# Kernel tuning notes

Hardware: AMD Instinct MI355X
Metric: run time of the kernel (lower is better)

The kernel has to match this reference:

```python
import jax, jax.numpy as jnp
import numpy as np

N = 50000      # nodes
E = 800000     # edges (before self loops)
H = 8          # heads in first n_layer-1 GATConv layers
C = 16         # per-head channels (hidden/heads)
HID = 128      # hidden_channels
IN = 128       # in_dim
OUT = 10       # out_dim
G = 64         # number of graphs in batch
EPS = 1e-5     # BatchNorm eps
SLOPE = 0.2    # GATConv leaky_relu negative slope


def _gat_conv(x, src, dst, W, att_src, att_dst, bias, heads, ch):
    # x: [N, HID]; W: [HID, heads*ch]; att_*: [heads, ch]; bias: [heads*ch]
    h = (x @ W).reshape(N, heads, ch)                       # [N, h, c]
    a_src = jnp.sum(h * att_src, axis=-1)                   # [N, h]
    a_dst = jnp.sum(h * att_dst, axis=-1)                   # [N, h]
    e = jax.nn.leaky_relu(a_src[src] + a_dst[dst], SLOPE)   # [E', h]
    # numerically stable segment softmax over incoming edges of each dst node
    e = e - jax.ops.segment_max(e, dst, num_segments=N)[dst]
    ee = jnp.exp(e)
    denom = jax.ops.segment_sum(ee, dst, num_segments=N)[dst]
    alpha = ee / denom                                      # [E', h]
    out = jax.ops.segment_sum(h[src] * alpha[..., None], dst, num_segments=N)
    return out.reshape(N, heads * ch) + bias                # [N, heads*ch]


def _bn(x, gamma, beta):
    # PyG BatchNorm in training mode: batch stats over node dim (biased var)
    m = jnp.mean(x, axis=0)
    v = jnp.var(x, axis=0)
    return (x - m) * jax.lax.rsqrt(v + EPS) * gamma + beta


def setup_inputs() -> dict:
    key = jax.random.key(0)
    ks = jax.random.split(key, 24)
    s = 0.05
    inp = {
        "x": jax.random.normal(ks[0], (N, IN), jnp.float32),
        "edge_index": jax.random.randint(ks[1], (2, E), 0, N, jnp.int64),
        "cycle_index": jax.random.randint(ks[2], (2, 1000), 0, N, jnp.int64),
        "batch": jnp.sort(jax.random.randint(ks[3], (N,), 0, G, jnp.int64)),
        "W_emb": jax.random.normal(ks[4], (IN, HID), jnp.float32) * s,
        "b_emb": jnp.zeros((HID,), jnp.float32),
        "conv_W": jax.random.normal(ks[5], (2, HID, H * C), jnp.float32) * s,
        "conv_att_src": jax.random.normal(ks[6], (2, H, C), jnp.float32) * s,
        "conv_att_dst": jax.random.normal(ks[7], (2, H, C), jnp.float32) * s,
        "conv_b": jnp.zeros((2, H * C), jnp.float32),
        "conv2_W": jax.random.normal(ks[8], (HID, HID), jnp.float32) * s,
        "conv2_att_src": jax.random.normal(ks[9], (1, HID), jnp.float32) * s,
        "conv2_att_dst": jax.random.normal(ks[10], (1, HID), jnp.float32) * s,
        "conv2_b": jnp.zeros((HID,), jnp.float32),
        "bn_gamma": jnp.ones((3, HID), jnp.float32),
        "bn_beta": jnp.zeros((3, HID), jnp.float32),
        "lin1_W": jax.random.normal(ks[11], (HID, HID), jnp.float32) * s,
        "lin1_b": jnp.zeros((HID,), jnp.float32),
        "lin2_W": jax.random.normal(ks[12], (HID, HID), jnp.float32) * s,
        "lin2_b": jnp.zeros((HID,), jnp.float32),
        "lin3_W": jax.random.normal(ks[13], (HID, OUT), jnp.float32) * s,
        "lin3_b": jnp.zeros((OUT,), jnp.float32),
    }
    return inp


def reference(x, edge_index, cycle_index, batch, W_emb, b_emb, conv_W,
              conv_att_src, conv_att_dst, conv_b, conv2_W, conv2_att_src,
              conv2_att_dst, conv2_b, bn_gamma, bn_beta, lin1_W, lin1_b,
              lin2_W, lin2_b, lin3_W, lin3_b):
    # GATConv default add_self_loops=True
    loops = jnp.arange(N, dtype=edge_index.dtype)
    src = jnp.concatenate([edge_index[0], loops])
    dst = jnp.concatenate([edge_index[1], loops])

    h = x @ W_emb + b_emb  # dropout(p=0) is identity
    for i in range(3):
        if i < 2:
            c = _gat_conv(h, src, dst, conv_W[i], conv_att_src[i],
                          conv_att_dst[i], conv_b[i], H, C)
        else:
            c = _gat_conv(h, src, dst, conv2_W, conv2_att_src,
                          conv2_att_dst, conv2_b, 1, HID)
        h = jax.nn.relu(_bn(c, bn_gamma[i], bn_beta[i])) + h

    # global mean pool over graphs
    sums = jax.ops.segment_sum(h, batch, num_segments=G)
    cnts = jax.ops.segment_sum(jnp.ones((N, 1), h.dtype), batch, num_segments=G)
    pooled = sums / jnp.maximum(cnts, 1.0)

    out = jax.nn.relu(pooled @ lin1_W + lin1_b)
    out = jax.nn.relu(out @ lin2_W + lin2_b)
    return out @ lin3_W + lin3_b
```

## Files before the change

### kernel.cpp

```cpp
#include <hip/hip_runtime.h>


#define NN   50000
#define NE   800000
#define NET  (NE + NN)
#define HD   128
#define NG   64
#define NB   196
#define NBN  391
#define NCH  20
#define NTILE 3321
#define PSZ  6250

typedef unsigned short u16;
typedef __attribute__((ext_vector_type(8))) short short8;
typedef __attribute__((ext_vector_type(4))) float f32x4;

#define O_WEMB 0
#define O_BEMB 16384
#define O_CW   16512
#define O_CAS  49280
#define O_CAD  49536
#define O_CB   49792
#define O_C2W  50048
#define O_C2AS 66432
#define O_C2AD 66560
#define O_C2B  66688
#define O_BNG  66816
#define O_BNB  67200
#define O_L1W  67584
#define O_L1B  83968
#define O_L2W  84096
#define O_L2B  100480
#define O_L3W  100608
#define O_L3B  101888
#define NPAR   101898

__device__ int   g_f32flag;
__device__ __align__(16) u16 g_x [NN*HD];
__device__ __align__(16) u16 g_par[NPAR];
__device__ int   g_src[NE], g_dst[NE], g_batch[NN];
__device__ __align__(16) float g_h[NN*HD];
__device__ __align__(16) u16 g_hb[NN*HD];
__device__ __align__(16) u16 g_hw[NN*HD];
__device__ __align__(16) u16 g_c[NN*HD];
__device__ float g_asrc[NN*8];
__device__ float g_adst[NN*8];
__device__ int   g_rowptr[NN+1];
__device__ int   g_cursor[NN];
__device__ int   g_bsum[NB], g_boff[NB];
__device__ int   g_csr[NET];
__device__ float g_bnp1[NBN*HD], g_bnp2[NBN*HD];
__device__ float g_scl[HD], g_shf[HD];
__device__ int   g_gcnt[NG], g_goff[NG];
__device__ __align__(16) float g_poolp[NG*NCH*HD];
__device__ __align__(16) u16 g_WT[4][HD*HD];

__device__ __forceinline__ float b2f(u16 u) {
    unsigned v = ((unsigned)u) << 16; float f; __builtin_memcpy(&f, &v, 4); return f;
}
__device__ __forceinline__ u16 f2b(float f) {
    unsigned v; __builtin_memcpy(&v, &f, 4);
    return (u16)((v + 0x7fffu + ((v >> 16) & 1u)) >> 16);
}

__device__ __forceinline__ int probe_f32(const void* xp) {
    const u16* p = (const u16*)xp;
    int ex = (p[threadIdx.x & 63] >> 7) & 0xff;
    return __ballot(ex >= 0x93) != 0ULL;
}
__device__ __forceinline__ int probe_i64(const void* eip) {
    const int* q = (const int*)eip;
    return __ballot(q[2*(threadIdx.x & 63) + 1] != 0) == 0ULL;
}

__device__ __forceinline__ int block_incl_scan(int v, int* lds4) {
    int t = threadIdx.x, lane = t & 63, w = t >> 6;
    #pragma unroll
    for (int d = 1; d < 64; d <<= 1) {
        int o = __shfl_up(v, d);
        if (lane >= d) v += o;
    }
    if (lane == 63) lds4[w] = v;
    __syncthreads();
    if (w == 0 && lane < 4) {
        int s = lds4[lane];
        #pragma unroll
        for (int d = 1; d < 4; d <<= 1) {
            int o = __shfl_up(s, d);
            if (lane >= d) s += o;
        }
        lds4[lane] = s;
    }
    __syncthreads();
    if (w > 0) v += lds4[w-1];
    return v;
}

__global__ void k_convx(const void* xp) {
    int gi = blockIdx.x*256 + threadIdx.x;
    int f32 = probe_f32(xp);
    if (gi == 0) g_f32flag = f32;
    if (gi < NN) g_cursor[gi] = 1;
    int i = gi*4;
    if (f32) {
        float4 v = *(const float4*)((const float*)xp + i);
        ushort4 o = { f2b(v.x), f2b(v.y), f2b(v.z), f2b(v.w) };
        *(ushort4*)&g_x[i] = o;
    } else {
        *(ushort4*)&g_x[i] = *(const ushort4*)((const u16*)xp + i);
    }
}
struct P18 { const void* p[18]; int off[18]; int n[18]; };
__global__ void k_convpar(P18 a, const void* xp) {
    int f32 = probe_f32(xp);
    for (int t = 0; t < 18; ++t) {
        const void* s = a.p[t]; int off = a.off[t], n = a.n[t];
        for (int i = blockIdx.x*256 + threadIdx.x; i < n; i += 64*256)
            g_par[off+i] = f32 ? f2b(((const float*)s)[i]) : ((const u16*)s)[i];
    }
}
__global__ void k_convidx(const void* ei, const void* ba) {
    int i64 = probe_i64(ei);
    int e = blockIdx.x*256 + threadIdx.x;
    if (e < NE) {
        int s, d;
        if (i64) { s = (int)((const long long*)ei)[e]; d = (int)((const long long*)ei)[NE + e]; }
        else     { s = ((const int*)ei)[e];            d = ((const int*)ei)[NE + e]; }
        g_src[e] = s; g_dst[e] = d;
        atomicAdd(&g_cursor[d], 1);
    }
    if (e < NN)
        g_batch[e] = i64 ? (int)((const long long*)ba)[e] : ((const int*)ba)[e];
}

__global__ void k_blocksum() {
    int i = blockIdx.x*256 + threadIdx.x;
    int v = (i < NN) ? g_cursor[i] : 0;
    #pragma unroll
    for (int d = 32; d; d >>= 1) v += __shfl_down(v, d);
    __shared__ int lds[4];
    if ((threadIdx.x & 63) == 0) lds[threadIdx.x >> 6] = v;
    __syncthreads();
    if (threadIdx.x == 0) g_bsum[blockIdx.x] = lds[0]+lds[1]+lds[2]+lds[3];
}
__global__ void k_misc() {
    int b = blockIdx.x;
    if (b < 256) {
        int which = b >> 6;
        int poff = which==0 ? O_WEMB : which==1 ? O_CW : which==2 ? (O_CW+16384) : O_C2W;
        int idx = (b & 63)*256 + threadIdx.x;
        int n = idx >> 7, k = idx & 127;
        g_WT[which][n*HD + k] = g_par[poff + k*HD + n];
    } else if (b == 256) {
        __shared__ int lds[4];
        int t = threadIdx.x;
        int v = (t < NB) ? g_bsum[t] : 0;
        int incl = block_incl_scan(v, lds);
        if (t < NB) g_boff[t] = incl - v;
    } else {
        __shared__ int off[NG+1];
        int g = threadIdx.x;
        if (g <= NG) {
            int lo = 0, hi = NN;
            while (lo < hi) { int mid = (lo+hi) >> 1; if (g_batch[mid] < g) lo = mid+1; else hi = mid; }
            off[g] = lo;
        }
        __syncthreads();
        if (g < NG) { g_goff[g] = off[g]; g_gcnt[g] = off[g+1] - off[g]; }
    }
}
__global__ void k_downsweep() {
    __shared__ int lds[4];
    int i = blockIdx.x*256 + threadIdx.x;
    int c = (i < NN) ? g_cursor[i] : 0;
    int incl = block_incl_scan(c, lds);
    int base = g_boff[blockIdx.x];
    if (i < NN) {
        g_rowptr[i+1] = base + incl;
        g_cursor[i]   = base + incl - c;
    }
    if (i == 0) g_rowptr[0] = 0;
}

__global__ void k_scatter() {
    int part = blockIdx.x & 7;
    int e = (blockIdx.x >> 3)*256 + threadIdx.x;
    if (e >= NET) return;
    int s, d;
    if (e < NE) { s = g_src[e]; d = g_dst[e]; } else { s = d = e - NE; }
    if (d / PSZ != part) return;
    int pos = atomicAdd(&g_cursor[d], 1);
    g_csr[pos] = s;
}

__global__ __launch_bounds__(256) void k_gemm(int asel, int wsel, int biasoff,
                                              int outmode, int nrows,
                                              int asoff, int adoff, int heads,
                                              int bnfuse) {
    __shared__ __align__(16) u16 wt[HD*136];
    __shared__ float s_scl[HD], s_shf[HD];
    const u16* A = asel ? g_hb : g_x;
    const u16* WTg = g_WT[wsel];
    int t = threadIdx.x;
    #pragma unroll
    for (int i = 0; i < 8; ++i) {
        int e = (t + i*256) * 8;
        int n = e >> 7, k = e & 127;
        *(uint4*)&wt[n*136 + k] = *(const uint4*)&WTg[e];
    }
    if (bnfuse && t < HD) { s_scl[t] = g_scl[t]; s_shf[t] = g_shf[t]; }
    __syncthreads();
    int lane = t & 63, wave = t >> 6;
    int m16 = lane & 15, q = lane >> 4;
    int row0 = blockIdx.x*128 + wave*32;
    f32x4 acc[2][8];
    #pragma unroll
    for (int a = 0; a < 2; ++a)
        #pragma unroll
        for (int b = 0; b < 8; ++b) acc[a][b] = (f32x4){0.f,0.f,0.f,0.f};
    #pragma unroll
    for (int kc = 0; kc < 4; ++kc) {
        short8 af[2];
        #pragma unroll
        for (int rt = 0; rt < 2; ++rt) {
            int r = row0 + rt*16 + m16; if (r > nrows-1) r = nrows-1;
            int base = r*HD + kc*32 + q*8;
            if (bnfuse) {
                short8 cv = *(const short8*)&g_c[base];
                float4 h0 = *(const float4*)&g_h[base];
                float4 h1 = *(const float4*)&g_h[base+4];
                float nh[8];
                #pragma unroll
                for (int k2 = 0; k2 < 8; ++k2) {
                    int ch = kc*32 + q*8 + k2;
                    float hv = (k2 < 4) ? (&h0.x)[k2] : (&h1.x)[k2-4];
                    float v = fmaxf(b2f((u16)cv[k2])*s_scl[ch] + s_shf[ch], 0.f) + hv;
                    nh[k2] = v;
                    af[rt][k2] = (short)f2b(v);
                }
                float4 o0 = {nh[0],nh[1],nh[2],nh[3]};
                float4 o1 = {nh[4],nh[5],nh[6],nh[7]};
                *(float4*)&g_h[base]   = o0;
                *(float4*)&g_h[base+4] = o1;
            } else {
                af[rt] = *(const short8*)&A[base];
            }
        }
        #pragma unroll
        for (int ct = 0; ct < 8; ++ct) {
            short8 bf = *(const short8*)&wt[(ct*16 + m16)*136 + kc*32 + q*8];
            acc[0][ct] = __builtin_amdgcn_mfma_f32_16x16x32_bf16(af[0], bf, acc[0][ct], 0,0,0);
            acc[1][ct] = __builtin_amdgcn_mfma_f32_16x16x32_bf16(af[1], bf, acc[1][ct], 0,0,0);
        }
    }
    #pragma unroll
    for (int rt = 0; rt < 2; ++rt)
        #pragma unroll
        for (int reg = 0; reg < 4; ++reg) {
            int r = row0 + rt*16 + q*4 + reg;
            if (r < nrows) {
                #pragma unroll
                for (int ct = 0; ct < 8; ++ct) {
                    int c = ct*16 + m16;
                    float v = acc[rt][ct][reg];
                    if (biasoff >= 0) v += b2f(g_par[biasoff + c]);
                    if (outmode == 0) { g_h[r*HD+c] = v; g_hb[r*HD+c] = f2b(v); }
                    else              { g_hw[r*HD+c] = f2b(v); }
                }
            }
        }
    if (asoff >= 0) {
        #pragma unroll
        for (int rt = 0; rt < 2; ++rt)
            #pragma unroll
            for (int reg = 0; reg < 4; ++reg) {
                float v[8], u[8];
                #pragma unroll
                for (int ct = 0; ct < 8; ++ct) {
                    float w = acc[rt][ct][reg];
                    v[ct] = w * b2f(g_par[asoff + ct*16 + m16]);
                    u[ct] = w * b2f(g_par[adoff + ct*16 + m16]);
                }
                #pragma unroll
                for (int d = 1; d < 16; d <<= 1)
                    #pragma unroll
                    for (int ct = 0; ct < 8; ++ct) {
                        v[ct] += __shfl_xor(v[ct], d);
                        u[ct] += __shfl_xor(u[ct], d);
                    }
                int r = row0 + rt*16 + q*4 + reg;
                if (m16 == 0 && r < nrows) {
                    if (heads == 8) {
                        #pragma unroll
                        for (int h = 0; h < 8; ++h) {
                            g_asrc[r*8 + h] = v[h];
                            g_adst[r*8 + h] = u[h];
                        }
                    } else {
                        float sv = 0.f, su = 0.f;
                        #pragma unroll
                        for (int ct = 0; ct < 8; ++ct) { sv += v[ct]; su += u[ct]; }
                        g_asrc[r] = sv; g_adst[r] = su;
                    }
                }
            }
    }
}

__global__ __launch_bounds__(256) void k_flash(int boff, int heads, int hs) {
    int node = blockIdx.x*4 + (threadIdx.x >> 6);
    int lane = threadIdx.x & 63;
    int c0 = lane*2;
    int head = c0 >> hs;
    float ad = g_adst[node*heads + head];
    int beg = g_rowptr[node], end = g_rowptr[node+1];
    float l = 0.f, o0 = 0.f, o1 = 0.f;
    int j = beg;
    for (; j + 8 <= end; j += 8) {
        int s[8]; float av[8]; unsigned w[8];
        #pragma unroll
        for (int k = 0; k < 8; ++k) s[k] = g_csr[j+k];
        #pragma unroll
        for (int k = 0; k < 8; ++k) av[k] = g_asrc[s[k]*heads + head];
        #pragma unroll
        for (int k = 0; k < 8; ++k) w[k] = *(const unsigned*)&g_hw[s[k]*HD + c0];
        #pragma unroll
        for (int k = 0; k < 8; ++k) {
            float e = av[k] + ad;
            e = fmaxf(e, 0.2f*e);
            float p = __expf(fminf(e, 30.f));
            l  += p;
            o0 += p*b2f((u16)(w[k] & 0xffff));
            o1 += p*b2f((u16)(w[k] >> 16));
        }
    }
    for (; j + 4 <= end; j += 4) {
        int s[4]; float av[4]; unsigned w[4];
        #pragma unroll
        for (int k = 0; k < 4; ++k) s[k] = g_csr[j+k];
        #pragma unroll
        for (int k = 0; k < 4; ++k) av[k] = g_asrc[s[k]*heads + head];
        #pragma unroll
        for (int k = 0; k < 4; ++k) w[k] = *(const unsigned*)&g_hw[s[k]*HD + c0];
        #pragma unroll
        for (int k = 0; k < 4; ++k) {
            float e = av[k] + ad;
            e = fmaxf(e, 0.2f*e);
            float p = __expf(fminf(e, 30.f));
            l  += p;
            o0 += p*b2f((u16)(w[k] & 0xffff));
            o1 += p*b2f((u16)(w[k] >> 16));
        }
    }
    for (; j < end; ++j) {
        int s = g_csr[j];
        float e = g_asrc[s*heads + head] + ad;
        e = fmaxf(e, 0.2f*e);
        float p = __expf(fminf(e, 30.f));
        unsigned w = *(const unsigned*)&g_hw[s*HD + c0];
        l  += p;
        o0 += p*b2f((u16)(w & 0xffff));
        o1 += p*b2f((u16)(w >> 16));
    }
    float inv = 1.f/l;
    ushort2 o = { f2b(o0*inv + b2f(g_par[boff + c0])),
                  f2b(o1*inv + b2f(g_par[boff + c0 + 1])) };
    *(ushort2*)&g_c[node*HD + c0] = o;
}

__global__ void k_bnstats() {
    int t = threadIdx.x; int ch = t & 127, r0 = t >> 7;
    int base = blockIdx.x*128;
    float s = 0.f, q = 0.f;
    for (int i = r0; i < 128; i += 2) {
        int n = base + i;
        if (n < NN) { float v = b2f(g_c[n*HD + ch]); s += v; q += v*v; }
    }
    __shared__ float sS[256], sQ[256];
    sS[t] = s; sQ[t] = q; __syncthreads();
    if (t < 128) {
        g_bnp1[blockIdx.x*HD + t] = sS[t] + sS[t+128];
        g_bnp2[blockIdx.x*HD + t] = sQ[t] + sQ[t+128];
    }
}
__global__ void k_bnfinal(int goff, int boff) {
    int ch = blockIdx.x, t = threadIdx.x;
    float s = 0.f, q = 0.f;
    for (int b = t; b < NBN; b += 64) { s += g_bnp1[b*HD + ch]; q += g_bnp2[b*HD + ch]; }
    #pragma unroll
    for (int d = 32; d; d >>= 1) { s += __shfl_down(s, d); q += __shfl_down(q, d); }
    if (t == 0) {
        float mean = s / (float)NN;
        float var  = fmaxf(q / (float)NN - mean*mean, 0.f);
        float sc = b2f(g_par[goff + ch]) * rsqrtf(var + 1e-5f);
        g_scl[ch] = sc;
        g_shf[ch] = b2f(g_par[boff + ch]) - mean*sc;
    }
}

__global__ void k_pool() {
    int g = blockIdx.x / NCH, c = blockIdx.x - g*NCH;
    int cnt = g_gcnt[g], off = g_goff[g];
    int step = (cnt + NCH - 1) / NCH;
    int r0 = c*step, r1 = min(cnt, r0 + step);
    int t = threadIdx.x;
    int ch = (t & 31) * 4;
    int rr = t >> 5;
    float sc0 = g_scl[ch], sc1 = g_scl[ch+1], sc2 = g_scl[ch+2], sc3 = g_scl[ch+3];
    float sf0 = g_shf[ch], sf1 = g_shf[ch+1], sf2 = g_shf[ch+2], sf3 = g_shf[ch+3];
    float4 s = {0.f,0.f,0.f,0.f};
    for (int i = r0 + rr; i < r1; i += 8) {
        int base = (off + i)*HD + ch;
        ushort4 cv = *(const ushort4*)&g_c[base];
        float4 hv = *(const float4*)&g_h[base];
        s.x += fmaxf(b2f(cv.x)*sc0 + sf0, 0.f) + hv.x;
        s.y += fmaxf(b2f(cv.y)*sc1 + sf1, 0.f) + hv.y;
        s.z += fmaxf(b2f(cv.z)*sc2 + sf2, 0.f) + hv.z;
        s.w += fmaxf(b2f(cv.w)*sc3 + sf3, 0.f) + hv.w;
    }
    __shared__ float4 sh[256];
    sh[t] = s; __syncthreads();
    if (t < 32) {
        float4 a = sh[t];
        #pragma unroll
        for (int k = 1; k < 8; ++k) {
            float4 b = sh[t + k*32];
            a.x += b.x; a.y += b.y; a.z += b.z; a.w += b.w;
        }
        *(float4*)&g_poolp[(g*NCH + c)*HD + ch] = a;
    }
}

__global__ void k_head(void* outB) {
    __shared__ float pl[HD], h1[HD], h2[HD];
    int g = blockIdx.x, t = threadIdx.x;
    float s = 0.f;
    for (int c = 0; c < NCH; ++c) s += g_poolp[(g*NCH + c)*HD + t];
    pl[t] = s / fmaxf((float)g_gcnt[g], 1.f);
    __syncthreads();
    float acc = b2f(g_par[O_L1B + t]);
    for (int k = 0; k < HD; ++k) acc += pl[k] * b2f(g_par[O_L1W + k*HD + t]);
    h1[t] = fmaxf(acc, 0.f);
    __syncthreads();
    acc = b2f(g_par[O_L2B + t]);
    for (int k = 0; k < HD; ++k) acc += h1[k] * b2f(g_par[O_L2W + k*HD + t]);
    h2[t] = fmaxf(acc, 0.f);
    __syncthreads();
    if (t < 10) {
        acc = b2f(g_par[O_L3B + t]);
        for (int k = 0; k < HD; ++k) acc += h2[k] * b2f(g_par[O_L3W + k*10 + t]);
        if (g_f32flag) ((float*)outB)[g*10 + t] = acc;
        else           ((u16*)outB)[g*10 + t] = f2b(acc);
    }
}

extern "C" void kernel_launch(void* const* d_in, const int* in_sizes, int n_in,
                              void* d_out, int out_size, void* d_ws, size_t ws_size,
                              hipStream_t stream) {
    const void* x     = d_in[0];
    const void* ei    = d_in[1];
    const void* batch = d_in[3];

    k_convx<<<6250, 256, 0, stream>>>(x);
    P18 a;
    const int srcidx[18] = {4,5,6,7,8,9,10,11,12,13,14,15,16,17,18,19,20,21};
    const int offs[18] = {O_WEMB,O_BEMB,O_CW,O_CAS,O_CAD,O_CB,O_C2W,O_C2AS,O_C2AD,
                          O_C2B,O_BNG,O_BNB,O_L1W,O_L1B,O_L2W,O_L2B,O_L3W,O_L3B};
    const int lens[18] = {16384,128,32768,256,256,256,16384,128,128,128,384,384,
                          16384,128,16384,128,1280,10};
    for (int t = 0; t < 18; ++t) { a.p[t] = d_in[srcidx[t]]; a.off[t] = offs[t]; a.n[t] = lens[t]; }
    k_convpar<<<64, 256, 0, stream>>>(a, x);
    k_convidx<<<3125, 256, 0, stream>>>(ei, batch);

    k_blocksum<<<NB, 256, 0, stream>>>();
    k_misc<<<258, 256, 0, stream>>>();
    k_downsweep<<<NB, 256, 0, stream>>>();
    k_scatter<<<NTILE*8, 256, 0, stream>>>();

    k_gemm<<<391, 256, 0, stream>>>(0, 0, O_BEMB, 0, NN, -1, -1, 0, 0);

    for (int L = 0; L < 3; ++L) {
        int heads = (L < 2) ? 8 : 1;
        int hs    = (L < 2) ? 4 : 7;
        int as    = (L < 2) ? O_CAS + L*128 : O_C2AS;
        int ad    = (L < 2) ? O_CAD + L*128 : O_C2AD;
        int cb    = (L < 2) ? O_CB  + L*128 : O_C2B;
        k_gemm<<<391, 256, 0, stream>>>(1, L+1, -1, 1, NN, as, ad, heads, L > 0 ? 1 : 0);
        k_flash<<<12500, 256, 0, stream>>>(cb, heads, hs);
        k_bnstats<<<NBN, 256, 0, stream>>>();
        k_bnfinal<<<128, 64, 0, stream>>>(O_BNG + L*HD, O_BNB + L*HD);
    }

    k_pool<<<NG*NCH, 256, 0, stream>>>();
    k_head<<<NG, 128, 0, stream>>>(d_out);
}
```

Before: 552.9 us.

## Keep residual stream in bf16, merge param conversion kernel, defer src load

Removes the fp32 residual buffer g_h and keeps the running node features only in bf16 (g_hb). The fused BN+ReLU+residual step in the GEMM and the pooling kernel now read and write bf16. This halves residual memory traffic and drops the duplicate fp32 stores. It also folds the parameter conversion kernel into the input conversion kernel to save a launch, and loads src in the scatter kernel only after the partition check. Keeping the residual in bf16 adds rounding error that builds up across layers.

```diff
diff --git a/kernel.cpp b/kernel.cpp
--- a/kernel.cpp
+++ b/kernel.cpp
@@ -40,7 +40,6 @@
 __device__ __align__(16) u16 g_x [NN*HD];
 __device__ __align__(16) u16 g_par[NPAR];
 __device__ int   g_src[NE], g_dst[NE], g_batch[NN];
-__device__ __align__(16) float g_h[NN*HD];
 __device__ __align__(16) u16 g_hb[NN*HD];
 __device__ __align__(16) u16 g_hw[NN*HD];
 __device__ __align__(16) u16 g_c[NN*HD];
@@ -97,7 +96,8 @@
     return v;
 }
 
-__global__ void k_convx(const void* xp) {
+struct P18 { const void* p[18]; int off[18]; int n[18]; };
+__global__ void k_convx(const void* xp, P18 a) {
     int gi = blockIdx.x*256 + threadIdx.x;
     int f32 = probe_f32(xp);
     if (gi == 0) g_f32flag = f32;
@@ -110,14 +110,12 @@
     } else {
         *(ushort4*)&g_x[i] = *(const ushort4*)((const u16*)xp + i);
     }
-}
-struct P18 { const void* p[18]; int off[18]; int n[18]; };
-__global__ void k_convpar(P18 a, const void* xp) {
-    int f32 = probe_f32(xp);
-    for (int t = 0; t < 18; ++t) {
-        const void* s = a.p[t]; int off = a.off[t], n = a.n[t];
-        for (int i = blockIdx.x*256 + threadIdx.x; i < n; i += 64*256)
-            g_par[off+i] = f32 ? f2b(((const float*)s)[i]) : ((const u16*)s)[i];
+    if (blockIdx.x < 64) {
+        for (int t = 0; t < 18; ++t) {
+            const void* s = a.p[t]; int off = a.off[t], n = a.n[t];
+            for (int j = blockIdx.x*256 + threadIdx.x; j < n; j += 64*256)
+                g_par[off+j] = f32 ? f2b(((const float*)s)[j]) : ((const u16*)s)[j];
+        }
     }
 }
 __global__ void k_convidx(const void* ei, const void* ba) {
@@ -187,9 +185,9 @@
     int part = blockIdx.x & 7;
     int e = (blockIdx.x >> 3)*256 + threadIdx.x;
     if (e >= NET) return;
-    int s, d;
-    if (e < NE) { s = g_src[e]; d = g_dst[e]; } else { s = d = e - NE; }
+    int d = (e < NE) ? g_dst[e] : e - NE;
     if (d / PSZ != part) return;
+    int s = (e < NE) ? g_src[e] : d;
     int pos = atomicAdd(&g_cursor[d], 1);
     g_csr[pos] = s;
 }
@@ -228,21 +226,15 @@
             int base = r*HD + kc*32 + q*8;
             if (bnfuse) {
                 short8 cv = *(const short8*)&g_c[base];
-                float4 h0 = *(const float4*)&g_h[base];
-                float4 h1 = *(const float4*)&g_h[base+4];
-                float nh[8];
+                short8 hv = *(const short8*)&g_hb[base];
                 #pragma unroll
                 for (int k2 = 0; k2 < 8; ++k2) {
                     int ch = kc*32 + q*8 + k2;
-                    float hv = (k2 < 4) ? (&h0.x)[k2] : (&h1.x)[k2-4];
-                    float v = fmaxf(b2f((u16)cv[k2])*s_scl[ch] + s_shf[ch], 0.f) + hv;
-                    nh[k2] = v;
+                    float v = fmaxf(b2f((u16)cv[k2])*s_scl[ch] + s_shf[ch], 0.f)
+                              + b2f((u16)hv[k2]);
                     af[rt][k2] = (short)f2b(v);
                 }
-                float4 o0 = {nh[0],nh[1],nh[2],nh[3]};
-                float4 o1 = {nh[4],nh[5],nh[6],nh[7]};
-                *(float4*)&g_h[base]   = o0;
-                *(float4*)&g_h[base+4] = o1;
+                *(short8*)&g_hb[base] = af[rt];
             } else {
                 af[rt] = *(const short8*)&A[base];
             }
@@ -265,8 +257,8 @@
                     int c = ct*16 + m16;
                     float v = acc[rt][ct][reg];
                     if (biasoff >= 0) v += b2f(g_par[biasoff + c]);
-                    if (outmode == 0) { g_h[r*HD+c] = v; g_hb[r*HD+c] = f2b(v); }
-                    else              { g_hw[r*HD+c] = f2b(v); }
+                    if (outmode == 0) g_hb[r*HD+c] = f2b(v);
+                    else              g_hw[r*HD+c] = f2b(v);
                 }
             }
         }
@@ -413,11 +405,11 @@
     for (int i = r0 + rr; i < r1; i += 8) {
         int base = (off + i)*HD + ch;
         ushort4 cv = *(const ushort4*)&g_c[base];
-        float4 hv = *(const float4*)&g_h[base];
-        s.x += fmaxf(b2f(cv.x)*sc0 + sf0, 0.f) + hv.x;
-        s.y += fmaxf(b2f(cv.y)*sc1 + sf1, 0.f) + hv.y;
-        s.z += fmaxf(b2f(cv.z)*sc2 + sf2, 0.f) + hv.z;
-        s.w += fmaxf(b2f(cv.w)*sc3 + sf3, 0.f) + hv.w;
+        ushort4 hv = *(const ushort4*)&g_hb[base];
+        s.x += fmaxf(b2f(cv.x)*sc0 + sf0, 0.f) + b2f(hv.x);
+        s.y += fmaxf(b2f(cv.y)*sc1 + sf1, 0.f) + b2f(hv.y);
+        s.z += fmaxf(b2f(cv.z)*sc2 + sf2, 0.f) + b2f(hv.z);
+        s.w += fmaxf(b2f(cv.w)*sc3 + sf3, 0.f) + b2f(hv.w);
     }
     __shared__ float4 sh[256];
     sh[t] = s; __syncthreads();
@@ -462,7 +454,6 @@
     const void* ei    = d_in[1];
     const void* batch = d_in[3];
 
-    k_convx<<<6250, 256, 0, stream>>>(x);
     P18 a;
     const int srcidx[18] = {4,5,6,7,8,9,10,11,12,13,14,15,16,17,18,19,20,21};
     const int offs[18] = {O_WEMB,O_BEMB,O_CW,O_CAS,O_CAD,O_CB,O_C2W,O_C2AS,O_C2AD,
@@ -470,7 +461,8 @@
     const int lens[18] = {16384,128,32768,256,256,256,16384,128,128,128,384,384,
                           16384,128,16384,128,1280,10};
     for (int t = 0; t < 18; ++t) { a.p[t] = d_in[srcidx[t]]; a.off[t] = offs[t]; a.n[t] = lens[t]; }
-    k_convpar<<<64, 256, 0, stream>>>(a, x);
+
+    k_convx<<<6250, 256, 0, stream>>>(x, a);
     k_convidx<<<3125, 256, 0, stream>>>(ei, batch);
 
     k_blocksum<<<NB, 256, 0, stream>>>();
```

After: 536.3 us. 3.0% less time.
